# Optimization experiments

Measured on AMD Instinct MI355X. Metric: run time of the kernel, lower is better.

Reference implementation:

```python
import jax, jax.numpy as jnp
import numpy as np

N = 131072          # total instances
G = 2048            # n_groups
MAX = 128           # padded max group size (>= true max by construction)
E = 256             # embed_dim
H = 8               # num_heads
D = E // H          # head dim


def setup_inputs() -> dict:
    key = jax.random.key(0)
    ks = jax.random.split(key, 9)
    # every group id appears at least once (matches torch.unique-derived groups)
    gids = jnp.concatenate([
        jnp.arange(G, dtype=jnp.int32),
        jax.random.randint(ks[0], (N - G,), 0, G, dtype=jnp.int32),
    ])
    return {
        "tree_preds": jax.random.normal(ks[1], (N, E), dtype=jnp.float32),
        "group_ids": gids,
        "query": jax.random.normal(ks[2], (1, 1, E), dtype=jnp.float32) * 0.02,
        "w_in": jax.random.normal(ks[3], (3 * E, E), dtype=jnp.float32) * 0.02,
        "b_in": jax.random.normal(ks[4], (3 * E,), dtype=jnp.float32) * 0.02,
        "w_out": jax.random.normal(ks[5], (E, E), dtype=jnp.float32) * 0.02,
        "b_out": jax.random.normal(ks[6], (E,), dtype=jnp.float32) * 0.02,
        "w_lin": jax.random.normal(ks[7], (1, E), dtype=jnp.float32) * 0.02,
        "b_lin": jax.random.normal(ks[8], (1,), dtype=jnp.float32) * 0.02,
    }


def _forward(tree_preds, group_ids, query, w_in, b_in, w_out, b_out, w_lin, b_lin):
    # --- scatter ragged groups into padded [G, MAX, E] tensor ---
    sorter = jnp.argsort(group_ids)                   # stable instance sorter
    sorted_gid = group_ids[sorter]
    sizes = jax.ops.segment_sum(jnp.ones_like(group_ids), group_ids,
                                num_segments=G)       # [G] group sizes
    offsets = jnp.cumsum(sizes) - sizes               # exclusive cumsum
    pos = jnp.arange(N, dtype=sizes.dtype) - offsets[sorted_gid]  # slot in group
    embs = jnp.zeros((G, MAX, E), dtype=tree_preds.dtype)
    embs = embs.at[sorted_gid, pos].set(tree_preds[sorter])
    kp_mask = jnp.arange(MAX)[None, :] >= sizes[:, None]          # [G, MAX] True=pad

    # --- single-query multi-head attention pooling ---
    wq, wk, wv = w_in[:E], w_in[E:2 * E], w_in[2 * E:]
    bq, bk, bv = b_in[:E], b_in[E:2 * E], b_in[2 * E:]
    q = (query.reshape(E) @ wq.T + bq).reshape(H, D)              # shared query
    k = (embs @ wk.T + bk).reshape(G, MAX, H, D)
    v = (embs @ wv.T + bv).reshape(G, MAX, H, D)
    scores = jnp.einsum("hd,gmhd->ghm", q, k) / jnp.sqrt(jnp.float32(D))
    scores = jnp.where(kp_mask[:, None, :], -jnp.inf, scores)
    attn = jax.nn.softmax(scores, axis=-1)                        # [G, H, MAX]
    pooled = jnp.einsum("ghm,gmhd->ghd", attn, v).reshape(G, E)
    pooled = pooled @ w_out.T + b_out                             # out_proj
    return pooled @ w_lin.T + b_lin                               # [G, 1]


def reference(tree_preds, group_ids, query, w_in, b_in, w_out, b_out, w_lin, b_lin):
    return _forward(tree_preds, group_ids, query, w_in, b_in,
                    w_out, b_out, w_lin, b_lin)
```

## Files before the change

kernel.cpp:

```cpp
#include <hip/hip_runtime.h>
#include <hip/hip_bf16.h>

#define EDIM 256
#define INV_SQRT_D 0.17677669529663688f
#define NREP 8

#define WS_QB   4096
#define WS_UB   4104
#define WS_C    4112
#define WB_BYTE_OFF 36864
#define ZM_BYTE_OFF 65536

typedef __attribute__((ext_vector_type(8))) short short8;
typedef __attribute__((ext_vector_type(4))) float f32x4;

__device__ __forceinline__ unsigned short f2bf(float f) {
  unsigned u = __float_as_uint(f);
  unsigned r = (u + 0x7fffu + ((u >> 16) & 1u)) >> 16;
  return (unsigned short)r;
}

__device__ __forceinline__ unsigned int cvt_pk_bf16(float a, float b) {
  __hip_bfloat162 t = __float22bfloat162_rn(float2{a, b});
  unsigned int u;
  __builtin_memcpy(&u, &t, 4);
  return u;
}

__global__ __launch_bounds__(256) void prep(
    const float* __restrict__ query, const float* __restrict__ w_in,
    const float* __restrict__ b_in, const float* __restrict__ w_out,
    const float* __restrict__ b_out, const float* __restrict__ b_lin,
    const float* __restrict__ w_lin, float* __restrict__ ws,
    unsigned short* __restrict__ wb, unsigned long long* __restrict__ zm,
    int nzm) {
  const int b = blockIdx.x, t = threadIdx.x;
  if (b < 8) {
    __shared__ float qh[32];
    {
      const int rl = t >> 3, sub = t & 7;
      const float4* wr = (const float4*)(w_in + (size_t)(b * 32 + rl) * EDIM + sub * 32);
      const float4* qr = (const float4*)(query + sub * 32);
      float p = 0.f;
#pragma unroll
      for (int f4 = 0; f4 < 8; ++f4) {
        const float4 w = wr[f4], q = qr[f4];
        p += w.x * q.x + w.y * q.y + w.z * q.z + w.w * q.w;
      }
      p += __shfl_xor(p, 1, 64);
      p += __shfl_xor(p, 2, 64);
      p += __shfl_xor(p, 4, 64);
      if (sub == 0) qh[rl] = p + b_in[b * 32 + rl];
    }
    __syncthreads();
    float a = 0.f;
#pragma unroll 8
    for (int d = 0; d < 32; ++d)
      a += qh[d] * w_in[(size_t)(EDIM + b * 32 + d) * EDIM + t];
    wb[b * EDIM + t] = f2bf(a * INV_SQRT_D);
    if (t < 64) {
      float s = (t < 32) ? qh[t] * b_in[EDIM + b * 32 + t] : 0.f;
#pragma unroll
      for (int m = 32; m >= 1; m >>= 1) s += __shfl_xor(s, m, 64);
      if (t == 0) ws[WS_QB + b] = s * INV_SQRT_D;
    }
  } else if (b < 16) {
    const int j = b - 8;
    __shared__ float uh[32];
    {
      const int dl = t >> 3, sub = t & 7;
      float p = 0.f;
#pragma unroll 8
      for (int f = sub * 32; f < sub * 32 + 32; ++f)
        p += w_lin[f] * w_out[(size_t)f * EDIM + j * 32 + dl];
      p += __shfl_xor(p, 1, 64);
      p += __shfl_xor(p, 2, 64);
      p += __shfl_xor(p, 4, 64);
      if (sub == 0) uh[dl] = p;
    }
    __syncthreads();
    float a = 0.f;
#pragma unroll 8
    for (int d = 0; d < 32; ++d)
      a += uh[d] * w_in[(size_t)(2 * EDIM + j * 32 + d) * EDIM + t];
    wb[(8 + j) * EDIM + t] = f2bf(a);
    if (t < 64) {
      float s = (t < 32) ? uh[t] * b_in[2 * EDIM + j * 32 + t] : 0.f;
#pragma unroll
      for (int m = 32; m >= 1; m >>= 1) s += __shfl_xor(s, m, 64);
      if (t == 0) ws[WS_UB + j] = s;
    }
  } else if (b == 16) {
    __shared__ float red[256];
    red[t] = w_lin[t] * b_out[t];
    __syncthreads();
    for (int off = 128; off >= 1; off >>= 1) {
      if (t < off) red[t] += red[t + off];
      __syncthreads();
    }
    if (t == 0) ws[WS_C] = red[0] + b_lin[0];
  } else {
    for (int k = (b - 17) * 256 + t; k < nzm; k += 16 * 256) zm[k] = 0ull;
  }
}

__global__ __launch_bounds__(256, 4) void main_mfma(
    const float* __restrict__ x, const int* __restrict__ gid,
    const float* __restrict__ ws, const unsigned short* __restrict__ wb,
    float* __restrict__ zmf, int g16, int n_items) {
  const int t = threadIdx.x;
  const int lane = t & 63;
  const int n = lane & 15, quad = lane >> 4;
  const int h = n & 7, isw = (n >> 3) & 1;

  short8 bfrag[8];
#pragma unroll
  for (int kc = 0; kc < 8; ++kc)
    bfrag[kc] = *(const short8*)(wb + n * EDIM + quad * 8 + kc * 32);

  const float qb = ws[WS_QB + h];
  const float ub = ws[WS_UB + h];

  float* __restrict__ zr = zmf + (size_t)(blockIdx.x & (NREP - 1)) * g16;

  const int wid = (int)(blockIdx.x * (blockDim.x >> 6) + (t >> 6));
  const int nw = (int)(gridDim.x * (blockDim.x >> 6));
  const int ntiles = (n_items + 15) >> 4;

  for (int tile = wid; tile < ntiles; tile += nw) {
    const int base = tile << 4;
    const float* rowp = x + (size_t)(base + n) * EDIM + quad * 8;
    f32x4 acc = {0.f, 0.f, 0.f, 0.f};
    int4 g4;
    if (base + 16 <= n_items) {
      g4 = *(const int4*)(gid + base + quad * 4);
#pragma unroll
      for (int kc = 0; kc < 8; ++kc) {
        const float4 v0 = *(const float4*)(rowp + kc * 32);
        const float4 v1 = *(const float4*)(rowp + kc * 32 + 4);
        union { short8 s; unsigned int u[4]; } a;
        a.u[0] = cvt_pk_bf16(v0.x, v0.y);
        a.u[1] = cvt_pk_bf16(v0.z, v0.w);
        a.u[2] = cvt_pk_bf16(v1.x, v1.y);
        a.u[3] = cvt_pk_bf16(v1.z, v1.w);
        acc = __builtin_amdgcn_mfma_f32_16x16x32_bf16(a.s, bfrag[kc], acc, 0, 0, 0);
      }
    } else {
      int gg[4];
#pragma unroll
      for (int r = 0; r < 4; ++r)
        gg[r] = (base + quad * 4 + r < n_items) ? gid[base + quad * 4 + r] : 0;
      g4.x = gg[0]; g4.y = gg[1]; g4.z = gg[2]; g4.w = gg[3];
      const bool live = (base + n < n_items);
#pragma unroll
      for (int kc = 0; kc < 8; ++kc) {
        float4 v0 = {0.f, 0.f, 0.f, 0.f}, v1 = {0.f, 0.f, 0.f, 0.f};
        if (live) {
          v0 = *(const float4*)(rowp + kc * 32);
          v1 = *(const float4*)(rowp + kc * 32 + 4);
        }
        union { short8 s; unsigned int u[4]; } a;
        a.u[0] = cvt_pk_bf16(v0.x, v0.y);
        a.u[1] = cvt_pk_bf16(v0.z, v0.w);
        a.u[2] = cvt_pk_bf16(v1.x, v1.y);
        a.u[3] = cvt_pk_bf16(v1.z, v1.w);
        acc = __builtin_amdgcn_mfma_f32_16x16x32_bf16(a.s, bfrag[kc], acc, 0, 0, 0);
      }
    }
#pragma unroll
    for (int r = 0; r < 4; ++r) {
      const float mine = acc[r];
      const float partner = __shfl_xor(mine, 8, 64);
      const float sv = (isw ? partner : mine) + qb;
      const float wv = (isw ? mine : partner) + ub;
      const float e = __expf(sv);
      const float val = isw ? e * wv : e;
      const int g = (r == 0) ? g4.x : (r == 1) ? g4.y : (r == 2) ? g4.z : g4.w;
      if (base + quad * 4 + r < n_items)
        atomicAdd(zr + ((size_t)g * 16 + h * 2 + isw), val);
    }
  }
}

__global__ __launch_bounds__(256) void finalize(
    const float* __restrict__ zmf, const float* __restrict__ ws,
    float* __restrict__ out, int G) {
  const int g = blockIdx.x * blockDim.x + threadIdx.x;
  if (g >= G) return;
  float zs[8], ms[8];
#pragma unroll
  for (int hh = 0; hh < 8; ++hh) { zs[hh] = 0.f; ms[hh] = 0.f; }
  const int g16 = G * 16;
#pragma unroll
  for (int rep = 0; rep < NREP; ++rep) {
    const float* row = zmf + (size_t)rep * g16 + (size_t)g * 16;
#pragma unroll
    for (int hh = 0; hh < 8; ++hh) {
      zs[hh] += row[hh * 2];
      ms[hh] += row[hh * 2 + 1];
    }
  }
  double acc = (double)ws[WS_C];
#pragma unroll
  for (int hh = 0; hh < 8; ++hh)
    acc += (double)ms[hh] / (double)zs[hh];
  out[g] = (float)acc;
}

__device__ __forceinline__ float dot16_reduce(const float4 (&W)[16],
                                              const float4 xv, const int lane) {
  float p[16];
#pragma unroll
  for (int j = 0; j < 16; ++j)
    p[j] = W[j].x * xv.x + W[j].y * xv.y + W[j].z * xv.z + W[j].w * xv.w;
#pragma unroll
  for (int j = 0; j < 8; ++j) {
    float send = (lane & 1) ? p[j] : p[j + 8];
    float keep = (lane & 1) ? p[j + 8] : p[j];
    p[j] = keep + __shfl_xor(send, 1, 64);
  }
#pragma unroll
  for (int j = 0; j < 4; ++j) {
    float send = (lane & 2) ? p[j] : p[j + 4];
    float keep = (lane & 2) ? p[j + 4] : p[j];
    p[j] = keep + __shfl_xor(send, 2, 64);
  }
#pragma unroll
  for (int j = 0; j < 2; ++j) {
    float send = (lane & 4) ? p[j] : p[j + 2];
    float keep = (lane & 4) ? p[j + 2] : p[j];
    p[j] = keep + __shfl_xor(send, 4, 64);
  }
  {
    float send = (lane & 8) ? p[0] : p[1];
    float keep = (lane & 8) ? p[1] : p[0];
    p[0] = keep + __shfl_xor(send, 8, 64);
  }
  p[0] += __shfl_xor(p[0], 16, 64);
  p[0] += __shfl_xor(p[0], 32, 64);
  return p[0];
}

__device__ __forceinline__ int bitrev4(const int l4) {
  return ((l4 & 1) << 3) | ((l4 & 2) << 1) | ((l4 & 4) >> 1) | ((l4 & 8) >> 3);
}

__global__ __launch_bounds__(256) void group_scan(
    const float* __restrict__ x, const int* __restrict__ gid,
    const float* __restrict__ query, const float* __restrict__ w_in,
    const float* __restrict__ b_in, const float* __restrict__ w_out,
    const float* __restrict__ b_out, const float* __restrict__ w_lin,
    const float* __restrict__ b_lin, float* __restrict__ out, int n_items) {
  const int g = blockIdx.x;
  const int t = threadIdx.x;
  __shared__ float Wl[16 * EDIM];
  __shared__ float querys[EDIM], wls[EDIM], qs[EDIM], us[EDIM];
  __shared__ float qbias[8], ubias[8], csh;
  __shared__ float part[4][16], sums[16];

  querys[t] = query[t];
  wls[t] = w_lin[t];
  __syncthreads();
  {
    float acc = 0.f;
    const float4* wr = (const float4*)(w_in + (size_t)t * EDIM);
    for (int f4 = 0; f4 < EDIM / 4; ++f4) {
      float4 wv = wr[f4];
      int f = f4 * 4;
      acc += wv.x * querys[f] + wv.y * querys[f + 1] + wv.z * querys[f + 2] + wv.w * querys[f + 3];
    }
    qs[t] = acc + b_in[t];
  }
  {
    float acc = 0.f;
    for (int f = 0; f < EDIM; ++f) acc += wls[f] * w_out[(size_t)f * EDIM + t];
    us[t] = acc;
  }
  __syncthreads();
  for (int j = 0; j < 8; ++j) {
    float a = 0.f;
    for (int d = 0; d < 32; ++d)
      a += qs[j * 32 + d] * w_in[(size_t)(EDIM + j * 32 + d) * EDIM + t];
    Wl[j * EDIM + t] = a * INV_SQRT_D;
  }
  for (int j = 0; j < 8; ++j) {
    float a = 0.f;
    for (int d = 0; d < 32; ++d)
      a += us[j * 32 + d] * w_in[(size_t)(2 * EDIM + j * 32 + d) * EDIM + t];
    Wl[(8 + j) * EDIM + t] = a;
  }
  if (t < 8) {
    float qb = 0.f, ub = 0.f;
    for (int d = 0; d < 32; ++d) {
      qb += qs[t * 32 + d] * b_in[EDIM + t * 32 + d];
      ub += us[t * 32 + d] * b_in[2 * EDIM + t * 32 + d];
    }
    qbias[t] = qb * INV_SQRT_D;
    ubias[t] = ub;
  }
  if (t == 0) {
    float c = b_lin[0];
    for (int f = 0; f < EDIM; ++f) c += wls[f] * b_out[f];
    csh = c;
  }
  __syncthreads();

  const int lane = t & 63;
  const int wave = t >> 6;
  float4 W[16];
#pragma unroll
  for (int j = 0; j < 16; ++j)
    W[j] = *(const float4*)(Wl + j * EDIM + lane * 4);
  const int jv = bitrev4(lane & 15);
  const int h = jv & 7;
  const int isw = (jv >> 3) & 1;
  const float bias_s = qbias[h];
  const float bias_w = ubias[h];

  float accv = 0.f;
  const int nchunk = (n_items + 63) >> 6;
  for (int c = wave; c < nchunk; c += 4) {
    const int i0 = c << 6;
    const int ii = i0 + lane;
    const int gi = (ii < n_items) ? gid[ii] : -1;
    unsigned long long mk = __ballot(gi == g);
    while (mk) {
      const int bpos = __ffsll(mk) - 1;
      mk &= mk - 1;
      const int i = i0 + bpos;
      const float4 xv = *(const float4*)(x + (size_t)i * EDIM + lane * 4);
      const float p0 = dot16_reduce(W, xv, lane);
      const float tpair = __shfl_xor(p0, 1, 64);
      const float sv = (isw ? tpair : p0) + bias_s;
      const float wv = (isw ? p0 : tpair) + bias_w;
      const float e = __expf(sv);
      accv += isw ? e * wv : e;
    }
  }
  if (lane < 16) part[wave][h * 2 + isw] = accv;
  __syncthreads();
  if (t < 16) sums[t] = part[0][t] + part[1][t] + part[2][t] + part[3][t];
  __syncthreads();
  if (t == 0) {
    double acc = (double)csh;
    for (int hh = 0; hh < 8; ++hh)
      acc += (double)sums[2 * hh + 1] / (double)sums[2 * hh];
    out[g] = (float)acc;
  }
}

extern "C" void kernel_launch(void* const* d_in, const int* in_sizes, int n_in,
                              void* d_out, int out_size, void* d_ws, size_t ws_size,
                              hipStream_t stream) {
  const float* tree_preds = (const float*)d_in[0];
  const int* group_ids = (const int*)d_in[1];
  const float* query = (const float*)d_in[2];
  const float* w_in = (const float*)d_in[3];
  const float* b_in = (const float*)d_in[4];
  const float* w_out = (const float*)d_in[5];
  const float* b_out = (const float*)d_in[6];
  const float* w_lin = (const float*)d_in[7];
  const float* b_lin = (const float*)d_in[8];
  float* out = (float*)d_out;

  const int N = in_sizes[1];
  const int G = out_size;

  const size_t needA = (size_t)ZM_BYTE_OFF + (size_t)NREP * G * 16 * 4;
  if (ws_size >= needA) {
    float* ws = (float*)d_ws;
    unsigned short* wb = (unsigned short*)((char*)d_ws + WB_BYTE_OFF);
    float* zmf = (float*)((char*)d_ws + ZM_BYTE_OFF);
    prep<<<33, 256, 0, stream>>>(query, w_in, b_in, w_out, b_out, b_lin, w_lin,
                                 ws, wb, (unsigned long long*)zmf, NREP * G * 8);
    main_mfma<<<1024, 256, 0, stream>>>(tree_preds, group_ids, ws, wb, zmf,
                                        G * 16, N);
    finalize<<<(G + 255) / 256, 256, 0, stream>>>(zmf, ws, out, G);
  } else {
    group_scan<<<G, 256, 0, stream>>>(tree_preds, group_ids, query, w_in, b_in,
                                      w_out, b_out, w_lin, b_lin, out, N);
  }
}
```

Before: 217.2 us.

## Fuse finalize into main kernel via grid-wide atomic barrier

Removes the separate finalize launch. Main blocks now signal completion on a global counter, spin until every block has arrived, and then each wave reduces one group's replicated accumulators and writes the output. The main grid is halved so that all blocks can be resident at once, which the spin barrier requires to avoid deadlock. This saves one kernel launch and its gap, but adds barrier spinning and leaves fewer waves available for the streaming phase.

```diff
diff --git a/kernel.cpp b/kernel.cpp
--- a/kernel.cpp
+++ b/kernel.cpp
@@ -4,10 +4,12 @@
 #define EDIM 256
 #define INV_SQRT_D 0.17677669529663688f
 #define NREP 8
+#define GRID_MAIN 512
 
 #define WS_QB   4096
 #define WS_UB   4104
 #define WS_C    4112
+#define WS_FLAG 4120
 #define WB_BYTE_OFF 36864
 #define ZM_BYTE_OFF 65536
 
@@ -25,6 +27,14 @@
   unsigned int u;
   __builtin_memcpy(&u, &t, 4);
   return u;
+}
+
+__device__ __forceinline__ double shfl_xor_dbl(double v, int m) {
+  union { double d; int i[2]; } u;
+  u.d = v;
+  u.i[0] = __shfl_xor(u.i[0], m, 64);
+  u.i[1] = __shfl_xor(u.i[1], m, 64);
+  return u.d;
 }
 
 __global__ __launch_bounds__(256) void prep(
@@ -33,7 +43,7 @@
     const float* __restrict__ b_out, const float* __restrict__ b_lin,
     const float* __restrict__ w_lin, float* __restrict__ ws,
     unsigned short* __restrict__ wb, unsigned long long* __restrict__ zm,
-    int nzm) {
+    unsigned* __restrict__ flag, int nzm) {
   const int b = blockIdx.x, t = threadIdx.x;
   if (b < 8) {
     __shared__ float qh[32];
@@ -99,6 +109,7 @@
       __syncthreads();
     }
     if (t == 0) ws[WS_C] = red[0] + b_lin[0];
+    if (t == 1) *flag = 0u;
   } else {
     for (int k = (b - 17) * 256 + t; k < nzm; k += 16 * 256) zm[k] = 0ull;
   }
@@ -107,7 +118,8 @@
 __global__ __launch_bounds__(256, 4) void main_mfma(
     const float* __restrict__ x, const int* __restrict__ gid,
     const float* __restrict__ ws, const unsigned short* __restrict__ wb,
-    float* __restrict__ zmf, int g16, int n_items) {
+    float* __restrict__ zmf, float* __restrict__ out,
+    unsigned* __restrict__ flag, int g16, int n_items, int G) {
   const int t = threadIdx.x;
   const int lane = t & 63;
   const int n = lane & 15, quad = lane >> 4;
@@ -120,6 +132,7 @@
 
   const float qb = ws[WS_QB + h];
   const float ub = ws[WS_UB + h];
+  const float c = ws[WS_C];
 
   float* __restrict__ zr = zmf + (size_t)(blockIdx.x & (NREP - 1)) * g16;
 
@@ -180,31 +193,39 @@
         atomicAdd(zr + ((size_t)g * 16 + h * 2 + isw), val);
     }
   }
-}
-
-__global__ __launch_bounds__(256) void finalize(
-    const float* __restrict__ zmf, const float* __restrict__ ws,
-    float* __restrict__ out, int G) {
-  const int g = blockIdx.x * blockDim.x + threadIdx.x;
-  if (g >= G) return;
-  float zs[8], ms[8];
-#pragma unroll
-  for (int hh = 0; hh < 8; ++hh) { zs[hh] = 0.f; ms[hh] = 0.f; }
-  const int g16 = G * 16;
-#pragma unroll
-  for (int rep = 0; rep < NREP; ++rep) {
-    const float* row = zmf + (size_t)rep * g16 + (size_t)g * 16;
-#pragma unroll
-    for (int hh = 0; hh < 8; ++hh) {
-      zs[hh] += row[hh * 2];
-      ms[hh] += row[hh * 2 + 1];
-    }
-  }
-  double acc = (double)ws[WS_C];
-#pragma unroll
-  for (int hh = 0; hh < 8; ++hh)
-    acc += (double)ms[hh] / (double)zs[hh];
-  out[g] = (float)acc;
+
+  __syncthreads();
+  if (t == 0) {
+    __threadfence();
+    __hip_atomic_fetch_add(flag, 1u, __ATOMIC_ACQ_REL, __HIP_MEMORY_SCOPE_AGENT);
+    while (__hip_atomic_load(flag, __ATOMIC_ACQUIRE, __HIP_MEMORY_SCOPE_AGENT)
+           < (unsigned)gridDim.x)
+      __builtin_amdgcn_s_sleep(1);
+  }
+  __syncthreads();
+
+  const int gpb = (G + (int)gridDim.x - 1) / (int)gridDim.x;
+  const int gl = t >> 6;
+  const int g = (int)blockIdx.x * gpb + gl;
+  if (gl < gpb && g < G) {
+    const int slot = lane & 15;
+    const int rp = lane >> 4;
+    float v = 0.f;
+#pragma unroll
+    for (int rep = rp; rep < NREP; rep += 4)
+      v += __hip_atomic_load(zmf + (size_t)rep * g16 + (size_t)g * 16 + slot,
+                             __ATOMIC_RELAXED, __HIP_MEMORY_SCOPE_AGENT);
+    v += __shfl_xor(v, 16, 64);
+    v += __shfl_xor(v, 32, 64);
+    const float partner = __shfl_xor(v, 1, 64);
+    double dr = 0.0;
+    if (lane < 16 && !(slot & 1))
+      dr = (double)partner / (double)v;
+    dr += shfl_xor_dbl(dr, 2);
+    dr += shfl_xor_dbl(dr, 4);
+    dr += shfl_xor_dbl(dr, 8);
+    if (lane == 0) out[g] = (float)((double)c + dr);
+  }
 }
 
 __device__ __forceinline__ float dot16_reduce(const float4 (&W)[16],
@@ -371,11 +392,12 @@
     float* ws = (float*)d_ws;
     unsigned short* wb = (unsigned short*)((char*)d_ws + WB_BYTE_OFF);
     float* zmf = (float*)((char*)d_ws + ZM_BYTE_OFF);
+    unsigned* flag = (unsigned*)((char*)d_ws + WS_FLAG * 4);
     prep<<<33, 256, 0, stream>>>(query, w_in, b_in, w_out, b_out, b_lin, w_lin,
-                                 ws, wb, (unsigned long long*)zmf, NREP * G * 8);
-    main_mfma<<<1024, 256, 0, stream>>>(tree_preds, group_ids, ws, wb, zmf,
-                                        G * 16, N);
-    finalize<<<(G + 255) / 256, 256, 0, stream>>>(zmf, ws, out, G);
+                                 ws, wb, (unsigned long long*)zmf, flag,
+                                 NREP * G * 8);
+    main_mfma<<<GRID_MAIN, 256, 0, stream>>>(tree_preds, group_ids, ws, wb, zmf,
+                                             out, flag, G * 16, N, G);
   } else {
     group_scan<<<G, 256, 0, stream>>>(tree_preds, group_ids, query, w_in, b_in,
                                       w_out, b_out, w_lin, b_lin, out, N);
```

Result: slower. 255.4 us (+17.6%).

## Counting-sort instances by group to aggregate atomics per wave

Applied to the files above, without the earlier changes.

Adds a counting-sort kernel that builds a permutation of instances grouped by group id, using a grid-wide spin barrier between the histogram and scatter phases. The main MFMA kernel then gathers rows through the permutation and pre-reduces the exp-weighted values of same-group rows within a wave, so each tile issues far fewer global atomics. The cost is an extra kernel with two passes over group ids, indirect row gathers that are less coalesced, and a grid barrier that assumes all 512 blocks are co-resident.

```diff
diff --git a/kernel.cpp b/kernel.cpp
--- a/kernel.cpp
+++ b/kernel.cpp
@@ -104,14 +104,70 @@
   }
 }
 
+__global__ __launch_bounds__(256, 4) void sortk(
+    const int* __restrict__ gid, unsigned* __restrict__ cnt,
+    unsigned* __restrict__ flag, unsigned* __restrict__ perm,
+    int* __restrict__ sgid, int n_items, int G) {
+  const int t = threadIdx.x;
+  const int stride = (int)gridDim.x * 256;
+  for (int i = (int)blockIdx.x * 256 + t; i < n_items; i += stride)
+    atomicAdd(&cnt[(size_t)gid[i] * 16], 1u);
+  __syncthreads();
+  if (t == 0) {
+    __threadfence();
+    __hip_atomic_fetch_add(flag, 1u, __ATOMIC_ACQ_REL, __HIP_MEMORY_SCOPE_AGENT);
+    while (__hip_atomic_load(flag, __ATOMIC_ACQUIRE, __HIP_MEMORY_SCOPE_AGENT)
+           < (unsigned)gridDim.x)
+      __builtin_amdgcn_s_sleep(1);
+  }
+  __syncthreads();
+  __shared__ unsigned lbase[2048];
+  __shared__ unsigned tsum[256];
+  unsigned c8[8];
+  unsigned s = 0;
+#pragma unroll
+  for (int j = 0; j < 8; ++j) {
+    const int g = t * 8 + j;
+    c8[j] = (g < G) ? __hip_atomic_load(&cnt[(size_t)g * 16], __ATOMIC_RELAXED,
+                                        __HIP_MEMORY_SCOPE_AGENT)
+                    : 0u;
+    s += c8[j];
+  }
+  tsum[t] = s;
+  __syncthreads();
+  for (int off = 1; off < 256; off <<= 1) {
+    unsigned v = (t >= off) ? tsum[t - off] : 0u;
+    __syncthreads();
+    tsum[t] += v;
+    __syncthreads();
+  }
+  unsigned run = tsum[t] - s;
+#pragma unroll
+  for (int j = 0; j < 8; ++j) {
+    const int g = t * 8 + j;
+    if (g < 2048) lbase[g] = run;
+    run += c8[j];
+  }
+  __syncthreads();
+  for (int i = (int)blockIdx.x * 256 + t; i < n_items; i += stride) {
+    const int g = gid[i];
+    const unsigned r = atomicAdd(&cnt[(size_t)g * 16 + 8], 1u);
+    const unsigned p = lbase[g] + r;
+    perm[p] = (unsigned)i;
+    sgid[p] = g;
+  }
+}
+
 __global__ __launch_bounds__(256, 4) void main_mfma(
-    const float* __restrict__ x, const int* __restrict__ gid,
-    const float* __restrict__ ws, const unsigned short* __restrict__ wb,
-    float* __restrict__ zmf, int g16, int n_items) {
+    const float* __restrict__ x, const unsigned* __restrict__ perm,
+    const int* __restrict__ sgid, const float* __restrict__ ws,
+    const unsigned short* __restrict__ wb, float* __restrict__ zmf,
+    int g16, int n_items) {
   const int t = threadIdx.x;
   const int lane = t & 63;
   const int n = lane & 15, quad = lane >> 4;
   const int h = n & 7, isw = (n >> 3) & 1;
+  const size_t slotoff = (size_t)(h * 2 + isw);
 
   short8 bfrag[8];
 #pragma unroll
@@ -129,44 +185,22 @@
 
   for (int tile = wid; tile < ntiles; tile += nw) {
     const int base = tile << 4;
-    const float* rowp = x + (size_t)(base + n) * EDIM + quad * 8;
+    const int myrow = base + n;
+    const unsigned idx = perm[myrow < n_items ? myrow : (n_items - 1)];
+    const float* rowp = x + (size_t)idx * EDIM + quad * 8;
     f32x4 acc = {0.f, 0.f, 0.f, 0.f};
-    int4 g4;
-    if (base + 16 <= n_items) {
-      g4 = *(const int4*)(gid + base + quad * 4);
-#pragma unroll
-      for (int kc = 0; kc < 8; ++kc) {
-        const float4 v0 = *(const float4*)(rowp + kc * 32);
-        const float4 v1 = *(const float4*)(rowp + kc * 32 + 4);
-        union { short8 s; unsigned int u[4]; } a;
-        a.u[0] = cvt_pk_bf16(v0.x, v0.y);
-        a.u[1] = cvt_pk_bf16(v0.z, v0.w);
-        a.u[2] = cvt_pk_bf16(v1.x, v1.y);
-        a.u[3] = cvt_pk_bf16(v1.z, v1.w);
-        acc = __builtin_amdgcn_mfma_f32_16x16x32_bf16(a.s, bfrag[kc], acc, 0, 0, 0);
-      }
-    } else {
-      int gg[4];
-#pragma unroll
-      for (int r = 0; r < 4; ++r)
-        gg[r] = (base + quad * 4 + r < n_items) ? gid[base + quad * 4 + r] : 0;
-      g4.x = gg[0]; g4.y = gg[1]; g4.z = gg[2]; g4.w = gg[3];
-      const bool live = (base + n < n_items);
-#pragma unroll
-      for (int kc = 0; kc < 8; ++kc) {
-        float4 v0 = {0.f, 0.f, 0.f, 0.f}, v1 = {0.f, 0.f, 0.f, 0.f};
-        if (live) {
-          v0 = *(const float4*)(rowp + kc * 32);
-          v1 = *(const float4*)(rowp + kc * 32 + 4);
-        }
-        union { short8 s; unsigned int u[4]; } a;
-        a.u[0] = cvt_pk_bf16(v0.x, v0.y);
-        a.u[1] = cvt_pk_bf16(v0.z, v0.w);
-        a.u[2] = cvt_pk_bf16(v1.x, v1.y);
-        a.u[3] = cvt_pk_bf16(v1.z, v1.w);
-        acc = __builtin_amdgcn_mfma_f32_16x16x32_bf16(a.s, bfrag[kc], acc, 0, 0, 0);
-      }
-    }
+#pragma unroll
+    for (int kc = 0; kc < 8; ++kc) {
+      const float4 v0 = *(const float4*)(rowp + kc * 32);
+      const float4 v1 = *(const float4*)(rowp + kc * 32 + 4);
+      union { short8 s; unsigned int u[4]; } a;
+      a.u[0] = cvt_pk_bf16(v0.x, v0.y);
+      a.u[1] = cvt_pk_bf16(v0.z, v0.w);
+      a.u[2] = cvt_pk_bf16(v1.x, v1.y);
+      a.u[3] = cvt_pk_bf16(v1.z, v1.w);
+      acc = __builtin_amdgcn_mfma_f32_16x16x32_bf16(a.s, bfrag[kc], acc, 0, 0, 0);
+    }
+    float v[4];
 #pragma unroll
     for (int r = 0; r < 4; ++r) {
       const float mine = acc[r];
@@ -174,10 +208,36 @@
       const float sv = (isw ? partner : mine) + qb;
       const float wv = (isw ? mine : partner) + ub;
       const float e = __expf(sv);
-      const float val = isw ? e * wv : e;
-      const int g = (r == 0) ? g4.x : (r == 1) ? g4.y : (r == 2) ? g4.z : g4.w;
-      if (base + quad * 4 + r < n_items)
-        atomicAdd(zr + ((size_t)g * 16 + h * 2 + isw), val);
+      v[r] = isw ? e * wv : e;
+    }
+    if (base + 16 <= n_items) {
+      const int4 g4 = *(const int4*)(sgid + base + quad * 4);
+      const int gf = __shfl(g4.x, 0, 64);
+      const int gt = __shfl(g4.w, 63, 64);
+      if (gf == gt) {
+        float ssum = v[0] + v[1] + v[2] + v[3];
+        ssum += __shfl_xor(ssum, 16, 64);
+        ssum += __shfl_xor(ssum, 32, 64);
+        if (quad == 0)
+          atomicAdd(zr + ((size_t)gf * 16 + slotoff), ssum);
+      } else {
+        float rs = v[0];
+        int rg = g4.x;
+        if (g4.y == rg) rs += v[1];
+        else { atomicAdd(zr + ((size_t)rg * 16 + slotoff), rs); rg = g4.y; rs = v[1]; }
+        if (g4.z == rg) rs += v[2];
+        else { atomicAdd(zr + ((size_t)rg * 16 + slotoff), rs); rg = g4.z; rs = v[2]; }
+        if (g4.w == rg) rs += v[3];
+        else { atomicAdd(zr + ((size_t)rg * 16 + slotoff), rs); rg = g4.w; rs = v[3]; }
+        atomicAdd(zr + ((size_t)rg * 16 + slotoff), rs);
+      }
+    } else {
+#pragma unroll
+      for (int r = 0; r < 4; ++r) {
+        const int pos = base + quad * 4 + r;
+        if (pos < n_items)
+          atomicAdd(zr + ((size_t)sgid[pos] * 16 + slotoff), v[r]);
+      }
     }
   }
 }
@@ -366,14 +426,28 @@
   const int N = in_sizes[1];
   const int G = out_size;
 
-  const size_t needA = (size_t)ZM_BYTE_OFF + (size_t)NREP * G * 16 * 4;
-  if (ws_size >= needA) {
+  const size_t zm_bytes = (size_t)NREP * G * 16 * 4;
+  const size_t cnt_off = (size_t)ZM_BYTE_OFF + zm_bytes;
+  const size_t cnt_bytes = (size_t)G * 16 * 4;
+  const size_t flag_off = cnt_off + cnt_bytes;
+  const size_t perm_off = (flag_off + 64 + 255) & ~(size_t)255;
+  const size_t sgid_off = (perm_off + (size_t)N * 4 + 255) & ~(size_t)255;
+  const size_t needA = sgid_off + (size_t)N * 4 + 64;
+  const int nzm64 = (int)((zm_bytes + cnt_bytes + 64) / 8);
+
+  if (ws_size >= needA && G <= 2048) {
     float* ws = (float*)d_ws;
     unsigned short* wb = (unsigned short*)((char*)d_ws + WB_BYTE_OFF);
     float* zmf = (float*)((char*)d_ws + ZM_BYTE_OFF);
+    unsigned* cnt = (unsigned*)((char*)d_ws + cnt_off);
+    unsigned* flag = (unsigned*)((char*)d_ws + flag_off);
+    unsigned* perm = (unsigned*)((char*)d_ws + perm_off);
+    int* sgid = (int*)((char*)d_ws + sgid_off);
+
     prep<<<33, 256, 0, stream>>>(query, w_in, b_in, w_out, b_out, b_lin, w_lin,
-                                 ws, wb, (unsigned long long*)zmf, NREP * G * 8);
-    main_mfma<<<1024, 256, 0, stream>>>(tree_preds, group_ids, ws, wb, zmf,
+                                 ws, wb, (unsigned long long*)zmf, nzm64);
+    sortk<<<512, 256, 0, stream>>>(group_ids, cnt, flag, perm, sgid, N, G);
+    main_mfma<<<1024, 256, 0, stream>>>(tree_preds, perm, sgid, ws, wb, zmf,
                                         G * 16, N);
     finalize<<<(G + 255) / 256, 256, 0, stream>>>(zmf, ws, out, G);
   } else {
```

Measured after the change: 262.7 us. +20.9%, slower.
